# Performance work log

Hardware: AMD Instinct MI355X
Metric: run time of the kernel (lower is better)

Reference implementation:

```python
import jax, jax.numpy as jnp
import numpy as np

POOLSCALE = 4  # HSA: avg-pool kernel/stride = (scale, scale*4)

def _avg_pool(x, kh, kw):
    # kernel == stride and dims divisible -> exact reshape-mean pooling
    B, C, H, W = x.shape
    return x.reshape(B, C, H // kh, kh, W // kw, kw).mean(axis=(3, 5))

def setup_inputs() -> dict:
    key = jax.random.key(0)
    k1, k2, k3 = jax.random.split(key, 3)
    shape = (4, 64, 192, 192)
    return {
        "K": jax.random.normal(k1, shape, dtype=jnp.float32),
        "Q": jax.random.normal(k2, shape, dtype=jnp.float32),
        "V": jax.random.normal(k3, shape, dtype=jnp.float32),
    }

def reference(K, Q, V):
    B, C, H, W = Q.shape
    kh, kw = POOLSCALE, POOLSCALE * 4
    Qp = Q.reshape(B, C, H * W).transpose(0, 2, 1)          # [B, HW, C]
    Kp = _avg_pool(K, kh, kw)                               # [B, C, h, w]
    Kp = Kp.reshape(B, C, -1)                               # [B, C, hw_p]
    Vp = _avg_pool(V, kh, kw).reshape(B, C, -1)             # [B, C, hw_p]
    scores = jnp.einsum('bnc,bcm->bnm', Qp, Kp)             # [B, HW, hw_p]
    attn = jax.nn.softmax(scores, axis=1)                   # softmax over query dim (dim=1), as in torch code
    out = jnp.einsum('bcm,bnm->bcn', Vp, attn)              # V_pie @ attn^T -> [B, C, HW]
    return out.reshape(B, C, H, W)
```

## Files before the change

kernel.cpp:

```cpp
#include <hip/hip_runtime.h>
#include <stdint.h>

#define BB 4
#define CC 64
#define HH 192
#define WW 192
#define HWN (HH*WW)
#define KH 4
#define KW 16
#define PW (WW/KW)
#define MP ((HH/KH)*(WW/KW))
#define MITER (MP/64)
#define NCHUNK (HWN/256)
#define SCALE_W 65536.0f
#define INV_SCALE (1.0f/65536.0f)

typedef _Float16 half8 __attribute__((ext_vector_type(8)));
typedef _Float16 half4 __attribute__((ext_vector_type(4)));
typedef float floatx4 __attribute__((ext_vector_type(4)));

static __device__ __forceinline__ void gload16(const void* g, void* l) {
  __builtin_amdgcn_global_load_lds((const __attribute__((address_space(1))) void*)g,
                                   (__attribute__((address_space(3))) void*)l, 16, 0, 0);
}
#define WAITCNT_VM(N) asm volatile("s_waitcnt vmcnt(" #N ")" ::: "memory")
#define WAITCNT_LGKM0 asm volatile("s_waitcnt lgkmcnt(0)" ::: "memory")


__global__ __launch_bounds__(256) void pool_kernel(
    const float* __restrict__ Kin, const float* __restrict__ Vin,
    _Float16* __restrict__ kptF, float* __restrict__ vp) {
  int t = blockIdx.x * 256 + threadIdx.x;
  const int total = BB * CC * MP;
  bool isV = t >= total;
  int idx = isV ? t - total : t;
  int m = idx % MP;
  int c = (idx / MP) % CC;
  int b = idx / (MP * CC);
  int mh = m / PW, mw = m % PW;
  const float* src = (isV ? Vin : Kin) + (((b * CC + c) * HH + mh * KH) * WW + mw * KW);
  float s = 0.f;
#pragma unroll
  for (int r = 0; r < KH; ++r) {
    const float4* row = (const float4*)(src + r * WW);
#pragma unroll
    for (int j = 0; j < KW / 4; ++j) {
      float4 v = row[j];
      s += v.x + v.y + v.z + v.w;
    }
  }
  s *= (1.0f / (KH * KW));
  if (isV) {
    vp[(b * CC + c) * MP + m] = s;
  } else {
    int mi = m >> 6, mloc = m & 63, l15 = mloc >> 2, mf = mloc & 3;
    int ks = c >> 5, lhi = (c >> 3) & 3, e = c & 7;
    int lane = lhi * 16 + l15;
    kptF[(((((b * MITER + mi) * 4 + mf) * 2 + ks)) * 64 + lane) * 8 + e] = (_Float16)s;
  }
}

__global__ __launch_bounds__(576) void colsum_kernel(
    const float* __restrict__ Q, const _Float16* __restrict__ kptF,
    float* __restrict__ part) {
  int b = blockIdx.y;
  int n0 = blockIdx.x * 256;
  int tid = threadIdx.x;
  int wv = tid / 64;
  int lane = tid & 63;
  int l15 = lane & 15, lhi = lane >> 4;

  const _Float16* kb = kptF + b * MITER * 8 * 512;
  half8 bfr[4][2];
#pragma unroll
  for (int mf = 0; mf < 4; ++mf)
#pragma unroll
    for (int ks = 0; ks < 2; ++ks)
      bfr[mf][ks] = *(const half8*)(kb + ((wv * 4 + mf) * 2 + ks) * 512 + lane * 8);

  const float* Qb = Q + b * CC * HWN;
  floatx4 zero = {0.f, 0.f, 0.f, 0.f};
  float s0 = 0.f, s1 = 0.f, s2 = 0.f, s3 = 0.f;

#pragma unroll
  for (int it = 0; it < 8; ++it) {
    int nr = n0 + it * 32 + l15;
    half8 af[2][2];
#pragma unroll
    for (int nf = 0; nf < 2; ++nf)
#pragma unroll
      for (int ks = 0; ks < 2; ++ks)
#pragma unroll
        for (int e = 0; e < 8; ++e)
          af[nf][ks][e] = (_Float16)Qb[(ks * 32 + lhi * 8 + e) * HWN + nr + nf * 16];

    floatx4 sacc[2][4];
#pragma unroll
    for (int nf = 0; nf < 2; ++nf)
#pragma unroll
      for (int mf = 0; mf < 4; ++mf) sacc[nf][mf] = zero;
    __builtin_amdgcn_s_setprio(1);
#pragma unroll
    for (int ks = 0; ks < 2; ++ks)
#pragma unroll
      for (int nf = 0; nf < 2; ++nf)
#pragma unroll
        for (int mf = 0; mf < 4; ++mf)
          sacc[nf][mf] = __builtin_amdgcn_mfma_f32_16x16x32_f16(
              af[nf][ks], bfr[mf][ks], sacc[nf][mf], 0, 0, 0);
    __builtin_amdgcn_s_setprio(0);

#pragma unroll
    for (int nf = 0; nf < 2; ++nf)
#pragma unroll
      for (int r = 0; r < 4; ++r) {
        s0 += __expf(sacc[nf][0][r]);
        s1 += __expf(sacc[nf][1][r]);
        s2 += __expf(sacc[nf][2][r]);
        s3 += __expf(sacc[nf][3][r]);
      }
  }

  s0 += __shfl_xor(s0, 16); s0 += __shfl_xor(s0, 32);
  s1 += __shfl_xor(s1, 16); s1 += __shfl_xor(s1, 32);
  s2 += __shfl_xor(s2, 16); s2 += __shfl_xor(s2, 32);
  s3 += __shfl_xor(s3, 16); s3 += __shfl_xor(s3, 32);
  if (lane < 16) {
    float* p = part + (b * NCHUNK + blockIdx.x) * MP + wv * 64 + l15 * 4;
    p[0] = s0; p[1] = s1; p[2] = s2; p[3] = s3;
  }
}

__global__ __launch_bounds__(256) void colsum_reduce_kernel(
    const float* __restrict__ part, float* __restrict__ colsum) {
  int t = blockIdx.x * 256 + threadIdx.x;
  int m = t % MP;
  int b = t / MP;
  const float* p = part + b * NCHUNK * MP + m;
  float a0 = 0.f, a1 = 0.f, a2 = 0.f, a3 = 0.f;
#pragma unroll 4
  for (int nc = 0; nc < NCHUNK; nc += 4) {
    a0 += p[(nc + 0) * MP];
    a1 += p[(nc + 1) * MP];
    a2 += p[(nc + 2) * MP];
    a3 += p[(nc + 3) * MP];
  }
  colsum[t] = (a0 + a1) + (a2 + a3);
}

__global__ __launch_bounds__(256) void wprep_kernel(
    const float* __restrict__ vp, const float* __restrict__ colsum,
    _Float16* __restrict__ wqF) {
  int t = blockIdx.x * 256 + threadIdx.x;
  int m = t % MP;
  int c = (t / MP) % CC;
  int b = t / (CC * MP);
  float w = vp[t] / colsum[b * MP + m] * SCALE_W;
  int cf = c >> 4, l15 = c & 15;
  int mi = m >> 6, mloc = m & 63;
  int ks = mloc >> 5, lhi = (mloc >> 3) & 3, e = mloc & 7;
  int lane = lhi * 16 + l15;
  wqF[((((b * MITER + mi) * 4 + cf) * 2 + ks) * 64 + lane) * 8 + e] = (_Float16)w;
}

__global__ __launch_bounds__(256, 2) void attn_main_kernel(
    const float* __restrict__ Q, const _Float16* __restrict__ kptF,
    const _Float16* __restrict__ wqF, float* __restrict__ out) {
  __shared__ char lds[3 * 16384 + 4 * 4096];
  char* stg = lds;
  int b = blockIdx.y;
  int n0 = blockIdx.x * 128;
  int tid = threadIdx.x;
  int wv = tid >> 6;
  int lane = tid & 63;
  int l15 = lane & 15, lhi = lane >> 4;
  char* eb = lds + 49152 + wv * 4096;

  const _Float16* kb = kptF + b * MITER * 8 * 512;
  const _Float16* wb = wqF + b * MITER * 8 * 512;

#define STAGE_A(tt, ss)                                                        \
  {                                                                            \
    int q0_ = wv * 4;                                                          \
    _Pragma("unroll") for (int j_ = 0; j_ < 4; ++j_) {                         \
      int q_ = q0_ + j_;                                                       \
      const _Float16* sp_ = (q_ < 8 ? kb + (tt) * 4096 + q_ * 512              \
                                    : wb + (tt) * 4096 + (q_ - 8) * 512) +     \
                            lane * 8;                                          \
      gload16(sp_, stg + (ss) * 16384 + q_ * 1024);                            \
    }                                                                          \
  }

  STAGE_A(0, 0);
  STAGE_A(1, 1);

  const float* Qb = Q + b * CC * HWN;
  int nrow = n0 + wv * 32 + l15;
  half8 afrag[2][2];
#pragma unroll
  for (int nf = 0; nf < 2; ++nf)
#pragma unroll
    for (int ks = 0; ks < 2; ++ks)
#pragma unroll
      for (int e = 0; e < 8; ++e)
        afrag[nf][ks][e] = (_Float16)Qb[(ks * 32 + lhi * 8 + e) * HWN + nrow + nf * 16];

  floatx4 zero = {0.f, 0.f, 0.f, 0.f};
  floatx4 oacc[4][2];
#pragma unroll
  for (int cf = 0; cf < 4; ++cf)
#pragma unroll
    for (int nf = 0; nf < 2; ++nf) oacc[cf][nf] = zero;

  WAITCNT_VM(4);
  __builtin_amdgcn_sched_barrier(0);
  __builtin_amdgcn_s_barrier();

#pragma unroll
  for (int mi = 0; mi < MITER; ++mi) {
    const int sc = mi % 3;
    const int spv = (mi + 2) % 3;

    if (mi >= 1) {
      if (mi <= 7) { WAITCNT_VM(4); } else { WAITCNT_VM(0); }
      __builtin_amdgcn_sched_barrier(0);
      __builtin_amdgcn_s_barrier();
    }

    half8 bfr[4][2];
#pragma unroll
    for (int mf = 0; mf < 4; ++mf)
#pragma unroll
      for (int ks = 0; ks < 2; ++ks)
        bfr[mf][ks] = *(const half8*)(stg + sc * 16384 + (mf * 2 + ks) * 1024 + lane * 16);
    half8 wfr[4][2];
    half8 ef[2][2];
    if (mi >= 1) {
#pragma unroll
      for (int cf = 0; cf < 4; ++cf)
#pragma unroll
        for (int ks = 0; ks < 2; ++ks)
          wfr[cf][ks] = *(const half8*)(stg + spv * 16384 + 8192 + (cf * 2 + ks) * 1024 + lane * 16);
#pragma unroll
      for (int nf = 0; nf < 2; ++nf)
#pragma unroll
        for (int ks = 0; ks < 2; ++ks) {
          int nl = nf * 16 + l15;
          int slot = (ks * 4 + lhi) ^ (nl & 7);
          ef[nf][ks] = *(const half8*)(eb + nl * 128 + (slot << 4));
        }
    }

    WAITCNT_LGKM0;
    __builtin_amdgcn_sched_barrier(0);
    __builtin_amdgcn_s_barrier();

    if (mi + 2 < MITER) STAGE_A(mi + 2, spv);

    floatx4 sacc[2][4];
#pragma unroll
    for (int nf = 0; nf < 2; ++nf)
#pragma unroll
      for (int mf = 0; mf < 4; ++mf) sacc[nf][mf] = zero;
    __builtin_amdgcn_s_setprio(1);
#pragma unroll
    for (int ks = 0; ks < 2; ++ks)
#pragma unroll
      for (int nf = 0; nf < 2; ++nf)
#pragma unroll
        for (int mf = 0; mf < 4; ++mf)
          sacc[nf][mf] = __builtin_amdgcn_mfma_f32_16x16x32_f16(
              afrag[nf][ks], bfr[mf][ks], sacc[nf][mf], 0, 0, 0);
    if (mi >= 1) {
#pragma unroll
      for (int ks = 0; ks < 2; ++ks)
#pragma unroll
        for (int cf = 0; cf < 4; ++cf)
#pragma unroll
          for (int nf = 0; nf < 2; ++nf)
            oacc[cf][nf] = __builtin_amdgcn_mfma_f32_16x16x32_f16(
                wfr[cf][ks], ef[nf][ks], oacc[cf][nf], 0, 0, 0);
    }
    __builtin_amdgcn_s_setprio(0);

#pragma unroll
    for (int nf = 0; nf < 2; ++nf)
#pragma unroll
      for (int r = 0; r < 4; ++r) {
        int nl = nf * 16 + lhi * 4 + r;
        half4 h;
#pragma unroll
        for (int mf = 0; mf < 4; ++mf) h[mf] = (_Float16)__expf(sacc[nf][mf][r]);
        int byte = nl * 128 + ((((l15 >> 1) ^ (nl & 7))) << 4) + ((l15 & 1) << 3);
        *(half4*)(eb + byte) = h;
      }
  }

  {
    half8 wfr[4][2];
#pragma unroll
    for (int cf = 0; cf < 4; ++cf)
#pragma unroll
      for (int ks = 0; ks < 2; ++ks)
        wfr[cf][ks] = *(const half8*)(stg + 2 * 16384 + 8192 + (cf * 2 + ks) * 1024 + lane * 16);
    half8 ef[2][2];
#pragma unroll
    for (int nf = 0; nf < 2; ++nf)
#pragma unroll
      for (int ks = 0; ks < 2; ++ks) {
        int nl = nf * 16 + l15;
        int slot = (ks * 4 + lhi) ^ (nl & 7);
        ef[nf][ks] = *(const half8*)(eb + nl * 128 + (slot << 4));
      }
    __builtin_amdgcn_s_setprio(1);
#pragma unroll
    for (int ks = 0; ks < 2; ++ks)
#pragma unroll
      for (int cf = 0; cf < 4; ++cf)
#pragma unroll
        for (int nf = 0; nf < 2; ++nf)
          oacc[cf][nf] = __builtin_amdgcn_mfma_f32_16x16x32_f16(
              wfr[cf][ks], ef[nf][ks], oacc[cf][nf], 0, 0, 0);
    __builtin_amdgcn_s_setprio(0);
  }

  float* ob = out + b * CC * HWN;
#pragma unroll
  for (int cf = 0; cf < 4; ++cf)
#pragma unroll
    for (int nf = 0; nf < 2; ++nf)
#pragma unroll
      for (int r = 0; r < 4; ++r) {
        int c = cf * 16 + lhi * 4 + r;
        int n = n0 + wv * 32 + nf * 16 + l15;
        ob[c * HWN + n] = oacc[cf][nf][r] * INV_SCALE;
      }
}

extern "C" void kernel_launch(void* const* d_in, const int* in_sizes, int n_in,
                              void* d_out, int out_size, void* d_ws, size_t ws_size,
                              hipStream_t stream) {
  const float* K = (const float*)d_in[0];
  const float* Q = (const float*)d_in[1];
  const float* V = (const float*)d_in[2];
  float* out = (float*)d_out;
  char* ws = (char*)d_ws;
  _Float16* kptF  = (_Float16*)(ws);
  float*    vp    = (float*)(ws + 294912);
  _Float16* wqF   = (_Float16*)(ws + 294912 + 589824);
  float*    colsum = (float*)(ws + 294912 + 589824 + 294912);
  float*    part  = out;

  pool_kernel<<<(2 * BB * CC * MP) / 256, 256, 0, stream>>>(K, V, kptF, vp);
  colsum_kernel<<<dim3(NCHUNK, BB), 576, 0, stream>>>(Q, kptF, part);
  colsum_reduce_kernel<<<(BB * MP) / 256, 256, 0, stream>>>(part, colsum);
  wprep_kernel<<<(BB * CC * MP) / 256, 256, 0, stream>>>(vp, colsum, wqF);
  attn_main_kernel<<<dim3(HWN / 128, BB), 256, 0, stream>>>(Q, kptF, wqF, out);
}
```

Baseline: 99.23 us.

## Pre-convert Q to fp16 fragment layout and split colsum across more blocks

Adds a qprep kernel that converts Q from fp32 into fp16 tiles already laid out as MFMA fragments in workspace. A new colsum kernel reads these fragments directly and assigns one wave per (chunk, m-iteration) pair, which spreads the exp-sum work over many more blocks than the old 576-thread-per-chunk kernel. The aim is to cut repeated fp32 Q loads and conversion inside colsum and to raise parallelism. The cost is an extra kernel launch plus a write and re-read of a fp16 copy of Q, and it only runs when the workspace is large enough; otherwise the old kernel is kept as a fallback.

```diff
diff --git a/kernel.cpp b/kernel.cpp
--- a/kernel.cpp
+++ b/kernel.cpp
@@ -12,6 +12,7 @@
 #define MP ((HH/KH)*(WW/KW))
 #define MITER (MP/64)
 #define NCHUNK (HWN/256)
+#define NBTOT (HWN/32)
 #define SCALE_W 65536.0f
 #define INV_SCALE (1.0f/65536.0f)
 
@@ -60,7 +61,97 @@
   }
 }
 
-__global__ __launch_bounds__(576) void colsum_kernel(
+__global__ __launch_bounds__(256) void qprep_kernel(
+    const float* __restrict__ Q, _Float16* __restrict__ qF) {
+  int t = blockIdx.x * 256 + threadIdx.x;
+  int chunk = t >> 6;
+  int lane = t & 63;
+  int nf = chunk & 1;
+  int ks = (chunk >> 1) & 1;
+  int idx = chunk >> 2;
+  int nb = idx % NBTOT;
+  int b = idx / NBTOT;
+  int c0 = ks * 32 + (lane >> 4) * 8;
+  int n = nb * 32 + nf * 16 + (lane & 15);
+  const float* Qb = Q + (b * CC + c0) * HWN + n;
+  half8 h;
+#pragma unroll
+  for (int e = 0; e < 8; ++e) h[e] = (_Float16)Qb[e * HWN];
+  *(half8*)(qF + chunk * 512 + lane * 8) = h;
+}
+
+__global__ __launch_bounds__(512) void colsum_qf_kernel(
+    const _Float16* __restrict__ qF, const _Float16* __restrict__ kptF,
+    float* __restrict__ part) {
+  int tid = threadIdx.x;
+  int lane = tid & 63;
+  int l15 = lane & 15;
+  int u = blockIdx.x * 8 + (tid >> 6);
+  int mi = u % 9;
+  int v = u / 9;
+  int b = v / NCHUNK;
+  int nc = v % NCHUNK;
+
+  const _Float16* kb = kptF + b * MITER * 8 * 512;
+  half8 bfr[4][2];
+#pragma unroll
+  for (int mf = 0; mf < 4; ++mf)
+#pragma unroll
+    for (int ks = 0; ks < 2; ++ks)
+      bfr[mf][ks] = *(const half8*)(kb + ((mi * 4 + mf) * 2 + ks) * 512 + lane * 8);
+
+  floatx4 zero = {0.f, 0.f, 0.f, 0.f};
+  float s0 = 0.f, s1 = 0.f, s2 = 0.f, s3 = 0.f;
+
+#pragma unroll
+  for (int it = 0; it < 8; ++it) {
+    int nb = nc * 8 + it;
+    const _Float16* qc = qF + (size_t)((b * NBTOT + nb) * 4) * 512 + lane * 8;
+    half8 af[2][2];
+#pragma unroll
+    for (int ks = 0; ks < 2; ++ks)
+#pragma unroll
+      for (int nf = 0; nf < 2; ++nf)
+        af[nf][ks] = *(const half8*)(qc + (ks * 2 + nf) * 512);
+
+    floatx4 sacc[2][4];
+#pragma unroll
+    for (int nf = 0; nf < 2; ++nf)
+#pragma unroll
+      for (int mf = 0; mf < 4; ++mf) sacc[nf][mf] = zero;
+    __builtin_amdgcn_s_setprio(1);
+#pragma unroll
+    for (int ks = 0; ks < 2; ++ks)
+#pragma unroll
+      for (int nf = 0; nf < 2; ++nf)
+#pragma unroll
+        for (int mf = 0; mf < 4; ++mf)
+          sacc[nf][mf] = __builtin_amdgcn_mfma_f32_16x16x32_f16(
+              af[nf][ks], bfr[mf][ks], sacc[nf][mf], 0, 0, 0);
+    __builtin_amdgcn_s_setprio(0);
+
+#pragma unroll
+    for (int nf = 0; nf < 2; ++nf)
+#pragma unroll
+      for (int r = 0; r < 4; ++r) {
+        s0 += __expf(sacc[nf][0][r]);
+        s1 += __expf(sacc[nf][1][r]);
+        s2 += __expf(sacc[nf][2][r]);
+        s3 += __expf(sacc[nf][3][r]);
+      }
+  }
+
+  s0 += __shfl_xor(s0, 16); s0 += __shfl_xor(s0, 32);
+  s1 += __shfl_xor(s1, 16); s1 += __shfl_xor(s1, 32);
+  s2 += __shfl_xor(s2, 16); s2 += __shfl_xor(s2, 32);
+  s3 += __shfl_xor(s3, 16); s3 += __shfl_xor(s3, 32);
+  if (lane < 16) {
+    float* p = part + (b * NCHUNK + nc) * MP + mi * 64 + l15 * 4;
+    p[0] = s0; p[1] = s1; p[2] = s2; p[3] = s3;
+  }
+}
+
+__global__ __launch_bounds__(576) void colsum_fb_kernel(
     const float* __restrict__ Q, const _Float16* __restrict__ kptF,
     float* __restrict__ part) {
   int b = blockIdx.y;
@@ -349,10 +440,18 @@
   float*    vp    = (float*)(ws + 294912);
   _Float16* wqF   = (_Float16*)(ws + 294912 + 589824);
   float*    colsum = (float*)(ws + 294912 + 589824 + 294912);
-  float*    part  = out;
+  const size_t QF_OFF = 1204224;
+  const size_t QF_BYTES = (size_t)BB * NBTOT * 4 * 512 * 2;
+  _Float16* qF = (_Float16*)(ws + QF_OFF);
+  float* part = out;
 
   pool_kernel<<<(2 * BB * CC * MP) / 256, 256, 0, stream>>>(K, V, kptF, vp);
-  colsum_kernel<<<dim3(NCHUNK, BB), 576, 0, stream>>>(Q, kptF, part);
+  if (ws_size >= QF_OFF + QF_BYTES) {
+    qprep_kernel<<<(BB * NBTOT * 4 * 64) / 256, 256, 0, stream>>>(Q, qF);
+    colsum_qf_kernel<<<(BB * NCHUNK * 9) / 8, 512, 0, stream>>>(qF, kptF, part);
+  } else {
+    colsum_fb_kernel<<<dim3(NCHUNK, BB), 576, 0, stream>>>(Q, kptF, part);
+  }
   colsum_reduce_kernel<<<(BB * MP) / 256, 256, 0, stream>>>(part, colsum);
   wprep_kernel<<<(BB * CC * MP) / 256, 256, 0, stream>>>(vp, colsum, wqF);
   attn_main_kernel<<<dim3(HWN / 128, BB), 256, 0, stream>>>(Q, kptF, wqF, out);
```

Measured after the change: 88.37 us. 10.9% less time.
